# Kernel tuning notes

Measured on AMD Instinct MI355X. Metric: run time of the kernel, lower is better.

## Reference

```python
import jax, jax.numpy as jnp
import numpy as np

D_MODEL = 512
D_K = 64
D_V = 128
H = D_MODEL // D_V  # 4 heads (num_head = d_model // d_v per the source)
B, N = 4, 2048


def setup_inputs() -> dict:
    key = jax.random.key(0)
    k0, k1, k2, k3, k4 = jax.random.split(key, 5)
    s = 0.02
    return {
        "input_x": jax.random.normal(k0, (B, N, D_MODEL), jnp.float32),
        "Wq": jax.random.normal(k1, (D_MODEL, H * D_K), jnp.float32) * s,
        "Wk": jax.random.normal(k2, (D_MODEL, H * D_K), jnp.float32) * s,
        "Wv": jax.random.normal(k3, (D_MODEL, D_MODEL), jnp.float32) * s,
        "Wo": jax.random.normal(k4, (D_MODEL, D_MODEL), jnp.float32) * s,
    }


def reference(input_x, Wq, Wk, Wv, Wo):
    b, n, _ = input_x.shape
    # Contiguous per-head slices in the source == a simple reshape here.
    q = (input_x @ Wq).reshape(b, n, H, D_K)   # [B,N,H,dk]
    k = (input_x @ Wk).reshape(b, n, H, D_K)   # [B,N,H,dk]
    v = (input_x @ Wv).reshape(b, n, H, D_V)   # [B,N,H,dv]
    scale = jnp.sqrt(jnp.float32(D_K))
    scores = jnp.einsum('bqhd,bkhd->bhqk', q, k) / scale  # [B,H,N,N]
    # FAITHFUL quirk: the source uses nn.Softmax() with no dim on a 3D
    # (B,N,N) tensor; PyTorch's legacy dim inference picks dim=0 (batch).
    attn = jax.nn.softmax(scores, axis=0)
    out = jnp.einsum('bhqk,bkhd->bqhd', attn, v).reshape(b, n, H * D_V)
    return out @ Wo
```

## Files before the change

kernel.cpp:

```cpp
#include <hip/hip_runtime.h>
#include <hip/hip_bf16.h>


typedef __attribute__((ext_vector_type(8))) short short8;
typedef __attribute__((ext_vector_type(4))) float floatx4;
typedef unsigned short u16;
typedef unsigned int u32;

#define MFMA16(a, b, c) __builtin_amdgcn_mfma_f32_16x16x32_bf16((a), (b), (c), 0, 0, 0)

__device__ __forceinline__ u16 f2bf(float f) {
    union { float f; unsigned u; } v; v.f = f;
    unsigned r = v.u + 0x7fffu + ((v.u >> 16) & 1u);
    return (u16)(r >> 16);
}

__device__ __forceinline__ float bf2f(u16 b) {
    union { unsigned u; float f; } v; v.u = ((u32)b) << 16;
    return v.f;
}

__device__ __forceinline__ u32 pk2bf(float a, float b) {
#if __has_builtin(__builtin_amdgcn_cvt_pk_bf16_f32)
    typedef __attribute__((ext_vector_type(2))) __bf16 bf16x2;
    union { bf16x2 v; u32 u; } c;
    c.v = __builtin_amdgcn_cvt_pk_bf16_f32(a, b);
    return c.u;
#else
    return (u32)f2bf(a) | ((u32)f2bf(b) << 16);
#endif
}

__device__ __forceinline__ float ex2(float x) {
#if __has_builtin(__builtin_amdgcn_exp2f)
    return __builtin_amdgcn_exp2f(x);
#else
    return exp2f(x);
#endif
}

__device__ __forceinline__ void gload_lds16(const u16* g, u16* l) {
    __builtin_amdgcn_global_load_lds(
        (const __attribute__((address_space(1))) void*)(const void*)g,
        (__attribute__((address_space(3))) void*)(void*)l, 16, 0, 0);
}

__global__ __launch_bounds__(256) void cast_x_kernel(const float* __restrict__ x,
                                                     u16* __restrict__ xb) {
    int i = blockIdx.x * 256 + threadIdx.x;
    float4 v = ((const float4*)x)[i];
    ushort4 o;
    o.x = f2bf(v.x); o.y = f2bf(v.y); o.z = f2bf(v.z); o.w = f2bf(v.w);
    ((ushort4*)xb)[i] = o;
}

__global__ __launch_bounds__(256) void prep_w_kernel(
    const float* __restrict__ Wq, const float* __restrict__ Wk,
    const float* __restrict__ Wv, const float* __restrict__ Wo,
    u16* __restrict__ WallT, u16* __restrict__ WoT) {
    int i = blockIdx.x * 256 + threadIdx.x;
    if (i < 524288) {
        int n = i >> 9, k = i & 511;
        float v;
        if (n < 256)      v = Wq[k * 256 + n] * 0.18033688011f;
        else if (n < 512) v = Wk[k * 256 + (n - 256)];
        else              v = Wv[k * 512 + (n - 512)];
        WallT[i] = f2bf(v);
    } else {
        int j = i - 524288;
        int n = j >> 9, k = j & 511;
        WoT[j] = f2bf(Wo[k * 512 + n]);
    }
}

__global__ __launch_bounds__(256) void gemm_kernel(
    const u16* __restrict__ A, const u16* __restrict__ BT,
    float* __restrict__ Cf, u16* __restrict__ Qp, u16* __restrict__ Kp,
    u16* __restrict__ Vp, int Kdim, int ldc, int mode) {
    __shared__ u16 sm[16896];
    u16* Asl = sm;
    u16* Bsl = sm + 8192;
    const int tid = threadIdx.x;
    const int mbase = blockIdx.y * 128;
    const int nbase = blockIdx.x * 128;
    const int wave = tid >> 6, lane = tid & 63;
    const int wm = wave >> 1, wn = wave & 1;
    const int lq = lane & 15, quad = lane >> 4;

    const u16* gA = A + (size_t)(mbase + wave * 32 + (lane >> 3)) * Kdim + (lane & 7) * 8;
    const u16* gB = BT + (size_t)(nbase + wave * 32 + (lane >> 3)) * Kdim + (lane & 7) * 8;
    u16* lA = &Asl[(wave * 32) * 64];
    u16* lB = &Bsl[(wave * 32) * 64];

    const floatx4 z4 = {0.f, 0.f, 0.f, 0.f};
    floatx4 acc[4][4];
#pragma unroll
    for (int i = 0; i < 4; i++)
#pragma unroll
        for (int j = 0; j < 4; j++) acc[i][j] = z4;

    const int nk = Kdim >> 6;
    for (int kk = 0; kk < nk; kk++) {
        const int kb = kk << 6;
        if (kk) __syncthreads();
#pragma unroll
        for (int i = 0; i < 4; i++) {
            gload_lds16(gA + kb + (size_t)(i * 8) * Kdim, lA + (i * 8) * 64);
            gload_lds16(gB + kb + (size_t)(i * 8) * Kdim, lB + (i * 8) * 64);
        }
        __syncthreads();
#pragma unroll
        for (int ki = 0; ki < 2; ki++) {
            short8 af[4], bf[4];
#pragma unroll
            for (int mi = 0; mi < 4; mi++)
                af[mi] = *(const short8*)&Asl[(wm * 64 + mi * 16 + lq) * 64 + ki * 32 + quad * 8];
#pragma unroll
            for (int ni = 0; ni < 4; ni++)
                bf[ni] = *(const short8*)&Bsl[(wn * 64 + ni * 16 + lq) * 64 + ki * 32 + quad * 8];
#pragma unroll
            for (int mi = 0; mi < 4; mi++)
#pragma unroll
                for (int ni = 0; ni < 4; ni++)
                    acc[mi][ni] = MFMA16(af[mi], bf[ni], acc[mi][ni]);
        }
    }
    if (mode == 1) {
#pragma unroll
        for (int mi = 0; mi < 4; mi++)
#pragma unroll
            for (int ni = 0; ni < 4; ni++)
#pragma unroll
                for (int r = 0; r < 4; r++)
                    Cf[(size_t)(mbase + wm * 64 + mi * 16 + quad * 4 + r) * ldc +
                       (nbase + wn * 64 + ni * 16 + lq)] = acc[mi][ni][r];
        return;
    }
    __syncthreads();
    const bool vtile = (nbase >= 512);
#pragma unroll
    for (int mi = 0; mi < 4; mi++)
#pragma unroll
        for (int ni = 0; ni < 4; ni++) {
            int cl = wn * 64 + ni * 16 + lq;
#pragma unroll
            for (int r = 0; r < 4; r++) {
                int rl = wm * 64 + mi * 16 + quad * 4 + r;
                if (vtile) sm[cl * 132 + rl] = f2bf(acc[mi][ni][r]);
                else       sm[rl * 132 + cl] = f2bf(acc[mi][ni][r]);
            }
        }
    __syncthreads();
    const int b = mbase >> 11;
    const int keyb = mbase & 2047;
    if (nbase < 256) {
        const int hq = nbase >> 6;
        const int qs_base = keyb >> 4;
#pragma unroll
        for (int t = 0; t < 8; t++) {
            int l = wave * 8 + t;
            int qs2 = l >> 2, h2 = (l >> 1) & 1, ki = l & 1;
            int qd = lane >> 4, lqq = lane & 15;
            short8 v = *(const short8*)&sm[(qs2 * 16 + lqq) * 132 + h2 * 64 + ki * 32 + qd * 8];
            int h = hq + h2;
            size_t base = ((size_t)(((b * 4 + h) * 128 + (qs_base + qs2)) * 2 + ki) * 64 + lane) << 3;
            *(short8*)&Qp[base] = v;
        }
    } else if (nbase < 512) {
        const int hb = (nbase - 256) >> 6;
        const int ktb = keyb >> 6;
#pragma unroll
        for (int t = 0; t < 8; t++) {
            int l = wave * 8 + t;
            int kt2 = l >> 4, hf = (l >> 3) & 1, nj = (l >> 2) & 1;
            int h2 = (l >> 1) & 1, ki = l & 1;
            int quadk = lane >> 4, lqk = lane & 15;
            short8 v = *(const short8*)&sm[(kt2 * 64 + hf * 32 + lqk * 2 + nj) * 132 +
                                           h2 * 64 + ki * 32 + quadk * 8];
            int h = hb + h2;
            size_t base = ((size_t)(((((b * 4 + h) * 32 + (ktb + kt2)) * 2 + hf) * 2 + nj)
                                    * 2 + ki) * 64 + lane) << 3;
            *(short8*)&Kp[base] = v;
        }
    } else {
        const int h = (nbase - 512) >> 7;
        const int ktb = keyb >> 6;
#pragma unroll
        for (int t = 0; t < 8; t++) {
            int l = wave * 8 + t;
            int kt2 = l >> 4, hf = (l >> 3) & 1, niv = (l >> 1) & 3, wv = l & 1;
            int quadv = lane >> 4, lqv = lane & 15;
            short8 v = *(const short8*)&sm[(hf * 64 + niv * 16 + lqv) * 132 +
                                           kt2 * 64 + wv * 32 + quadv * 8];
            size_t base = ((size_t)(((((b * 4 + h) * 32 + (ktb + kt2)) * 2 + hf) * 4 + niv)
                                    * 2 + wv) * 64 + lane) << 3;
            *(short8*)&Vp[base] = v;
        }
    }
}

__global__ __launch_bounds__(512) void attn_kernel(const u16* __restrict__ Qp,
                                                   const u16* __restrict__ Kp,
                                                   const u16* __restrict__ Vp,
                                                   u16* __restrict__ Pp) {
    __shared__ u16 pl[2 * 4 * 4096];
    const int bx = blockIdx.x;
    const int h = bx & 3;
    const int ck = (bx >> 2) & 3;
    const int qt = bx >> 4;
    const int tid = threadIdx.x;
    const int wave = tid >> 6, lane = tid & 63;
    const int mi = wave & 3, half = wave >> 2;
    const int dq = wave;
    const int half_v = dq >> 2, ni_v = dq & 3;
    const int lq = lane & 15, quad = lane >> 4;
    const int qs = qt * 4 + mi;

    short8 aq[4][2];
#pragma unroll
    for (int b = 0; b < 4; b++)
#pragma unroll
        for (int ki = 0; ki < 2; ki++)
            aq[b][ki] = *(const short8*)&Qp[
                ((size_t)((((b * 4 + h) * 128 + qs) * 2 + ki) * 64 + lane) << 3)];

    const floatx4 z4 = {0.f, 0.f, 0.f, 0.f};
    floatx4 oacc[4][4];
#pragma unroll
    for (int b = 0; b < 4; b++)
#pragma unroll
        for (int m2 = 0; m2 < 4; m2++) oacc[b][m2] = z4;

    for (int kt = ck * 8; kt < ck * 8 + 8; kt++) {
        u16* plb = &pl[((kt & 1) * 4 + mi) * 4096];
        u16* plbuf = &pl[(kt & 1) * 4 * 4096];
        floatx4 s[4][2];
#pragma unroll
        for (int b = 0; b < 4; b++) {
            const u16* kb = Kp +
                ((size_t)((((b * 4 + h) * 32 + kt) * 2 + half) * 2) << 10) +
                lane * 8;
#pragma unroll
            for (int nj = 0; nj < 2; nj++) {
                s[b][nj] = z4;
#pragma unroll
                for (int ki = 0; ki < 2; ki++)
                    s[b][nj] = MFMA16(aq[b][ki],
                                      *(const short8*)(kb + (nj * 2 + ki) * 512),
                                      s[b][nj]);
            }
        }
        short8 vf[4][2];
#pragma unroll
        for (int b = 0; b < 4; b++) {
            const u16* vb = Vp +
                ((size_t)(((((b * 4 + h) * 32 + kt) * 2 + half_v) * 4 + ni_v) * 2) << 9) +
                lane * 8;
            vf[b][0] = *(const short8*)vb;
            vf[b][1] = *(const short8*)(vb + 512);
        }
#pragma unroll
        for (int r = 0; r < 4; r++) {
            float e0a = ex2(s[0][0][r]), e0b = ex2(s[0][1][r]);
            float e1a = ex2(s[1][0][r]), e1b = ex2(s[1][1][r]);
            float e2a = ex2(s[2][0][r]), e2b = ex2(s[2][1][r]);
            float e3a = ex2(s[3][0][r]), e3b = ex2(s[3][1][r]);
            float ia = __builtin_amdgcn_rcpf(e0a + e1a + e2a + e3a);
            float ib = __builtin_amdgcn_rcpf(e0b + e1b + e2b + e3b);
            int q = quad * 4 + r;
            int col = (half * 32 + 2 * lq) ^ ((q & 7) * 8);
            *(u32*)&plb[(0 * 16 + q) * 64 + col] = pk2bf(e0a * ia, e0b * ib);
            *(u32*)&plb[(1 * 16 + q) * 64 + col] = pk2bf(e1a * ia, e1b * ib);
            *(u32*)&plb[(2 * 16 + q) * 64 + col] = pk2bf(e2a * ia, e2b * ib);
            *(u32*)&plb[(3 * 16 + q) * 64 + col] = pk2bf(e3a * ia, e3b * ib);
        }
        __syncthreads();
        const int sw = (lq & 7) * 8;
#pragma unroll
        for (int b = 0; b < 4; b++) {
#pragma unroll
            for (int m2 = 0; m2 < 4; m2++) {
                const u16* pm = plbuf + m2 * 4096;
                short8 ap0 = *(const short8*)&pm[(b * 16 + lq) * 64 + ((quad * 8) ^ sw)];
                short8 ap1 = *(const short8*)&pm[(b * 16 + lq) * 64 + ((32 + quad * 8) ^ sw)];
                oacc[b][m2] = MFMA16(ap0, vf[b][0], oacc[b][m2]);
                oacc[b][m2] = MFMA16(ap1, vf[b][1], oacc[b][m2]);
            }
        }
    }
    u16* Pc = Pp + (size_t)ck * (8192 * 512);
#pragma unroll
    for (int b = 0; b < 4; b++)
#pragma unroll
        for (int m2 = 0; m2 < 4; m2++)
#pragma unroll
            for (int r = 0; r < 4; r++)
                Pc[(size_t)(b * 2048 + qt * 64 + m2 * 16 + quad * 4 + r) * 512 +
                   h * 128 + dq * 16 + lq] = f2bf(oacc[b][m2][r]);
}

__global__ __launch_bounds__(256) void reduce4_kernel(u16* __restrict__ P) {
    const size_t S = (size_t)8192 * 512;
    size_t i = ((size_t)blockIdx.x * 256 + threadIdx.x) * 8;
    short8 a = *(short8*)&P[i];
    short8 b = *(short8*)&P[i + S];
    short8 c = *(short8*)&P[i + 2 * S];
    short8 d = *(short8*)&P[i + 3 * S];
    short8 o;
#pragma unroll
    for (int j = 0; j < 8; j++) {
        float s = bf2f((u16)a[j]) + bf2f((u16)b[j]) +
                  bf2f((u16)c[j]) + bf2f((u16)d[j]);
        o[j] = (short)f2bf(s);
    }
    *(short8*)&P[i] = o;
}

extern "C" void kernel_launch(void* const* d_in, const int* in_sizes, int n_in,
                              void* d_out, int out_size, void* d_ws, size_t ws_size,
                              hipStream_t stream) {
    const float* x  = (const float*)d_in[0];
    const float* Wq = (const float*)d_in[1];
    const float* Wk = (const float*)d_in[2];
    const float* Wv = (const float*)d_in[3];
    const float* Wo = (const float*)d_in[4];
    float* out = (float*)d_out;

    char* ws = (char*)d_ws;
    u16* Pp    = (u16*)ws;
    u16* Xb    = (u16*)ws;
    u16* WallT = (u16*)(ws + (size_t)8 * 1024 * 1024);
    char* tail = ws + (size_t)32 * 1024 * 1024;
    u16* WoT   = (u16*)tail; tail += (size_t)512 * 512 * 2;
    u16* Qp    = (u16*)tail; tail += (size_t)8192 * 256 * 2;
    u16* Kp    = (u16*)tail; tail += (size_t)8192 * 256 * 2;
    u16* Vp    = (u16*)tail; tail += (size_t)8192 * 512 * 2;

    cast_x_kernel<<<4096, 256, 0, stream>>>(x, Xb);
    prep_w_kernel<<<3072, 256, 0, stream>>>(Wq, Wk, Wv, Wo, WallT, WoT);
    gemm_kernel<<<dim3(8, 64), 256, 0, stream>>>(Xb, WallT, nullptr,
                                                 Qp, Kp, Vp, 512, 0, 2);
    attn_kernel<<<512, 512, 0, stream>>>(Qp, Kp, Vp, Pp);
    reduce4_kernel<<<2048, 256, 0, stream>>>(Pp);
    gemm_kernel<<<dim3(4, 64), 256, 0, stream>>>(Pp, WoT, out,
                                                 nullptr, nullptr, nullptr,
                                                 512, 512, 1);
}
```

Before: 172.2 us.

## Merge prep kernels and retune QKV and output GEMMs to 512 threads

Merges the x cast and weight prep into one launch to save a kernel launch. The QKV GEMM moves from 256 to 512 threads per 128x128 tile, so each wave owns a 64x32 sub-tile. The output projection gets its own kernel with 64x128 tiles and 512 threads, doubling its block count to 512 for better CU coverage. The cost is fewer MFMAs per LDS fragment load and more waves sharing each barrier.

```diff
diff --git a/kernel.cpp b/kernel.cpp
--- a/kernel.cpp
+++ b/kernel.cpp
@@ -45,20 +45,21 @@
         (__attribute__((address_space(3))) void*)(void*)l, 16, 0, 0);
 }
 
-__global__ __launch_bounds__(256) void cast_x_kernel(const float* __restrict__ x,
-                                                     u16* __restrict__ xb) {
-    int i = blockIdx.x * 256 + threadIdx.x;
-    float4 v = ((const float4*)x)[i];
-    ushort4 o;
-    o.x = f2bf(v.x); o.y = f2bf(v.y); o.z = f2bf(v.z); o.w = f2bf(v.w);
-    ((ushort4*)xb)[i] = o;
-}
-
-__global__ __launch_bounds__(256) void prep_w_kernel(
+__global__ __launch_bounds__(256) void prep_all_kernel(
+    const float* __restrict__ x, u16* __restrict__ xb,
     const float* __restrict__ Wq, const float* __restrict__ Wk,
     const float* __restrict__ Wv, const float* __restrict__ Wo,
     u16* __restrict__ WallT, u16* __restrict__ WoT) {
-    int i = blockIdx.x * 256 + threadIdx.x;
+    int bid = blockIdx.x;
+    if (bid < 4096) {
+        int i = bid * 256 + threadIdx.x;
+        float4 v = ((const float4*)x)[i];
+        ushort4 o;
+        o.x = f2bf(v.x); o.y = f2bf(v.y); o.z = f2bf(v.z); o.w = f2bf(v.w);
+        ((ushort4*)xb)[i] = o;
+        return;
+    }
+    int i = (bid - 4096) * 256 + threadIdx.x;
     if (i < 524288) {
         int n = i >> 9, k = i & 511;
         float v;
@@ -73,10 +74,10 @@
     }
 }
 
-__global__ __launch_bounds__(256) void gemm_kernel(
+__global__ __launch_bounds__(512) void gemm_qkv_kernel(
     const u16* __restrict__ A, const u16* __restrict__ BT,
-    float* __restrict__ Cf, u16* __restrict__ Qp, u16* __restrict__ Kp,
-    u16* __restrict__ Vp, int Kdim, int ldc, int mode) {
+    u16* __restrict__ Qp, u16* __restrict__ Kp, u16* __restrict__ Vp,
+    int Kdim) {
     __shared__ u16 sm[16896];
     u16* Asl = sm;
     u16* Bsl = sm + 8192;
@@ -84,65 +85,54 @@
     const int mbase = blockIdx.y * 128;
     const int nbase = blockIdx.x * 128;
     const int wave = tid >> 6, lane = tid & 63;
-    const int wm = wave >> 1, wn = wave & 1;
+    const int wm = wave >> 2, wn = wave & 3;
     const int lq = lane & 15, quad = lane >> 4;
 
-    const u16* gA = A + (size_t)(mbase + wave * 32 + (lane >> 3)) * Kdim + (lane & 7) * 8;
-    const u16* gB = BT + (size_t)(nbase + wave * 32 + (lane >> 3)) * Kdim + (lane & 7) * 8;
-    u16* lA = &Asl[(wave * 32) * 64];
-    u16* lB = &Bsl[(wave * 32) * 64];
+    const u16* gA = A + (size_t)(mbase + wave * 16 + (lane >> 3)) * Kdim + (lane & 7) * 8;
+    const u16* gB = BT + (size_t)(nbase + wave * 16 + (lane >> 3)) * Kdim + (lane & 7) * 8;
+    u16* lA = &Asl[(wave * 16) * 64];
+    u16* lB = &Bsl[(wave * 16) * 64];
 
     const floatx4 z4 = {0.f, 0.f, 0.f, 0.f};
-    floatx4 acc[4][4];
+    floatx4 acc[4][2];
 #pragma unroll
     for (int i = 0; i < 4; i++)
 #pragma unroll
-        for (int j = 0; j < 4; j++) acc[i][j] = z4;
+        for (int j = 0; j < 2; j++) acc[i][j] = z4;
 
     const int nk = Kdim >> 6;
     for (int kk = 0; kk < nk; kk++) {
         const int kb = kk << 6;
         if (kk) __syncthreads();
 #pragma unroll
-        for (int i = 0; i < 4; i++) {
+        for (int i = 0; i < 2; i++) {
             gload_lds16(gA + kb + (size_t)(i * 8) * Kdim, lA + (i * 8) * 64);
             gload_lds16(gB + kb + (size_t)(i * 8) * Kdim, lB + (i * 8) * 64);
         }
         __syncthreads();
 #pragma unroll
         for (int ki = 0; ki < 2; ki++) {
-            short8 af[4], bf[4];
+            short8 af[4], bf[2];
 #pragma unroll
             for (int mi = 0; mi < 4; mi++)
                 af[mi] = *(const short8*)&Asl[(wm * 64 + mi * 16 + lq) * 64 + ki * 32 + quad * 8];
 #pragma unroll
-            for (int ni = 0; ni < 4; ni++)
-                bf[ni] = *(const short8*)&Bsl[(wn * 64 + ni * 16 + lq) * 64 + ki * 32 + quad * 8];
+            for (int ni = 0; ni < 2; ni++)
+                bf[ni] = *(const short8*)&Bsl[(wn * 32 + ni * 16 + lq) * 64 + ki * 32 + quad * 8];
 #pragma unroll
             for (int mi = 0; mi < 4; mi++)
 #pragma unroll
-                for (int ni = 0; ni < 4; ni++)
+                for (int ni = 0; ni < 2; ni++)
                     acc[mi][ni] = MFMA16(af[mi], bf[ni], acc[mi][ni]);
         }
-    }
-    if (mode == 1) {
-#pragma unroll
-        for (int mi = 0; mi < 4; mi++)
-#pragma unroll
-            for (int ni = 0; ni < 4; ni++)
-#pragma unroll
-                for (int r = 0; r < 4; r++)
-                    Cf[(size_t)(mbase + wm * 64 + mi * 16 + quad * 4 + r) * ldc +
-                       (nbase + wn * 64 + ni * 16 + lq)] = acc[mi][ni][r];
-        return;
     }
     __syncthreads();
     const bool vtile = (nbase >= 512);
 #pragma unroll
     for (int mi = 0; mi < 4; mi++)
 #pragma unroll
-        for (int ni = 0; ni < 4; ni++) {
-            int cl = wn * 64 + ni * 16 + lq;
+        for (int ni = 0; ni < 2; ni++) {
+            int cl = wn * 32 + ni * 16 + lq;
 #pragma unroll
             for (int r = 0; r < 4; r++) {
                 int rl = wm * 64 + mi * 16 + quad * 4 + r;
@@ -157,8 +147,8 @@
         const int hq = nbase >> 6;
         const int qs_base = keyb >> 4;
 #pragma unroll
-        for (int t = 0; t < 8; t++) {
-            int l = wave * 8 + t;
+        for (int t = 0; t < 4; t++) {
+            int l = wave * 4 + t;
             int qs2 = l >> 2, h2 = (l >> 1) & 1, ki = l & 1;
             int qd = lane >> 4, lqq = lane & 15;
             short8 v = *(const short8*)&sm[(qs2 * 16 + lqq) * 132 + h2 * 64 + ki * 32 + qd * 8];
@@ -170,8 +160,8 @@
         const int hb = (nbase - 256) >> 6;
         const int ktb = keyb >> 6;
 #pragma unroll
-        for (int t = 0; t < 8; t++) {
-            int l = wave * 8 + t;
+        for (int t = 0; t < 4; t++) {
+            int l = wave * 4 + t;
             int kt2 = l >> 4, hf = (l >> 3) & 1, nj = (l >> 2) & 1;
             int h2 = (l >> 1) & 1, ki = l & 1;
             int quadk = lane >> 4, lqk = lane & 15;
@@ -186,8 +176,8 @@
         const int h = (nbase - 512) >> 7;
         const int ktb = keyb >> 6;
 #pragma unroll
-        for (int t = 0; t < 8; t++) {
-            int l = wave * 8 + t;
+        for (int t = 0; t < 4; t++) {
+            int l = wave * 4 + t;
             int kt2 = l >> 4, hf = (l >> 3) & 1, niv = (l >> 1) & 3, wv = l & 1;
             int quadv = lane >> 4, lqv = lane & 15;
             short8 v = *(const short8*)&sm[(hf * 64 + niv * 16 + lqv) * 132 +
@@ -197,6 +187,64 @@
             *(short8*)&Vp[base] = v;
         }
     }
+}
+
+__global__ __launch_bounds__(512) void gemm_out_kernel(
+    const u16* __restrict__ A, const u16* __restrict__ BT,
+    float* __restrict__ Cf, int Kdim, int ldc) {
+    __shared__ u16 Asl[64 * 64];
+    __shared__ u16 Bsl[128 * 64];
+    const int tid = threadIdx.x;
+    const int mbase = blockIdx.y * 64;
+    const int nbase = blockIdx.x * 128;
+    const int wave = tid >> 6, lane = tid & 63;
+    const int wm = wave >> 2, wn = wave & 3;
+    const int lq = lane & 15, quad = lane >> 4;
+
+    const u16* gA = A + (size_t)(mbase + wave * 8 + (lane >> 3)) * Kdim + (lane & 7) * 8;
+    const u16* gB = BT + (size_t)(nbase + wave * 16 + (lane >> 3)) * Kdim + (lane & 7) * 8;
+    u16* lA = &Asl[(wave * 8) * 64];
+    u16* lB = &Bsl[(wave * 16) * 64];
+
+    const floatx4 z4 = {0.f, 0.f, 0.f, 0.f};
+    floatx4 acc[2][2];
+#pragma unroll
+    for (int i = 0; i < 2; i++)
+#pragma unroll
+        for (int j = 0; j < 2; j++) acc[i][j] = z4;
+
+    const int nk = Kdim >> 6;
+    for (int kk = 0; kk < nk; kk++) {
+        const int kb = kk << 6;
+        if (kk) __syncthreads();
+        gload_lds16(gA + kb, lA);
+        gload_lds16(gB + kb, lB);
+        gload_lds16(gB + kb + (size_t)8 * Kdim, lB + 8 * 64);
+        __syncthreads();
+#pragma unroll
+        for (int ki = 0; ki < 2; ki++) {
+            short8 af[2], bf[2];
+#pragma unroll
+            for (int mi = 0; mi < 2; mi++)
+                af[mi] = *(const short8*)&Asl[(wm * 32 + mi * 16 + lq) * 64 + ki * 32 + quad * 8];
+#pragma unroll
+            for (int ni = 0; ni < 2; ni++)
+                bf[ni] = *(const short8*)&Bsl[(wn * 32 + ni * 16 + lq) * 64 + ki * 32 + quad * 8];
+#pragma unroll
+            for (int mi = 0; mi < 2; mi++)
+#pragma unroll
+                for (int ni = 0; ni < 2; ni++)
+                    acc[mi][ni] = MFMA16(af[mi], bf[ni], acc[mi][ni]);
+        }
+    }
+#pragma unroll
+    for (int mi = 0; mi < 2; mi++)
+#pragma unroll
+        for (int ni = 0; ni < 2; ni++)
+#pragma unroll
+            for (int r = 0; r < 4; r++)
+                Cf[(size_t)(mbase + wm * 32 + mi * 16 + quad * 4 + r) * ldc +
+                   (nbase + wn * 32 + ni * 16 + lq)] = acc[mi][ni][r];
 }
 
 __global__ __launch_bounds__(512) void attn_kernel(const u16* __restrict__ Qp,
@@ -336,13 +384,9 @@
     u16* Kp    = (u16*)tail; tail += (size_t)8192 * 256 * 2;
     u16* Vp    = (u16*)tail; tail += (size_t)8192 * 512 * 2;
 
-    cast_x_kernel<<<4096, 256, 0, stream>>>(x, Xb);
-    prep_w_kernel<<<3072, 256, 0, stream>>>(Wq, Wk, Wv, Wo, WallT, WoT);
-    gemm_kernel<<<dim3(8, 64), 256, 0, stream>>>(Xb, WallT, nullptr,
-                                                 Qp, Kp, Vp, 512, 0, 2);
+    prep_all_kernel<<<7168, 256, 0, stream>>>(x, Xb, Wq, Wk, Wv, Wo, WallT, WoT);
+    gemm_qkv_kernel<<<dim3(8, 64), 512, 0, stream>>>(Xb, WallT, Qp, Kp, Vp, 512);
     attn_kernel<<<512, 512, 0, stream>>>(Qp, Kp, Vp, Pp);
     reduce4_kernel<<<2048, 256, 0, stream>>>(Pp);
-    gemm_kernel<<<dim3(4, 64), 256, 0, stream>>>(Pp, WoT, out,
-                                                 nullptr, nullptr, nullptr,
-                                                 512, 512, 1);
-}
+    gemm_out_kernel<<<dim3(4, 128), 512, 0, stream>>>(Pp, WoT, out, 512, 512);
+}
```

Result: faster. 166.7 us (-3.2%).
